# Performance work log

Measured on AMD Instinct MI355X. Metric: run time of the kernel, lower is better.

The kernel has to match this reference:

```python
import jax, jax.numpy as jnp
import numpy as np

D = 8        # q_ndim (= dof_ndim)
HID = 200    # hidden_size
N = 16384    # batch of states
EPS = 0.1    # qdot regularizer coefficient in L()


def _lagrangian(z, Ws, bs):
    # z: (2D,) = [q, qdot]; angular_dims=() so CosSin is an identity pass-through
    v = z[D:]
    h = z
    for W, b in zip(Ws[:-1], bs[:-1]):
        h = jax.nn.softplus(h @ W + b)   # FCsoftplus blocks
    L = (h @ Ws[-1] + bs[-1])[0]          # final Linear -> scalar (Reshape(-1))
    return L + EPS * jnp.dot(v, v)


def setup_inputs():
    key = jax.random.key(0)
    ks = jax.random.split(key, 5)
    z = jax.random.normal(ks[0], (N, 2 * D), dtype=jnp.float32)
    t = jnp.zeros((), dtype=jnp.float32)

    def lin(k, fi, fo, scale):
        return (jax.random.normal(k, (fi, fo), dtype=jnp.float32)
                * jnp.float32(scale / np.sqrt(fi)))

    W0 = lin(ks[1], 2 * D, HID, 1.0)
    W1 = lin(ks[2], HID, HID, 1.0)
    W2 = lin(ks[3], HID, HID, 1.0)
    W3 = lin(ks[4], HID, 1, 0.01)  # small head keeps mass matrix M well conditioned
    b0 = jnp.zeros((HID,), jnp.float32)  # zero_bias init per FCsoftplus/Linear
    b1 = jnp.zeros((HID,), jnp.float32)
    b2 = jnp.zeros((HID,), jnp.float32)
    b3 = jnp.zeros((1,), jnp.float32)
    return dict(t=t, z=z, W0=W0, b0=b0, W1=W1, b1=b1, W2=W2, b2=b2, W3=W3, b3=b3)


def reference(t, z, W0, b0, W1, b1, W2, b2, W3, b3):
    # Euler-Lagrange dynamics (LagrangianDynamics):
    #   M a = dL/dq - (d2L/dq dv) v,  M = d2L/dv2;  dz/dt = [v, a]
    Ws = (W0, W1, W2, W3)
    bs = (b0, b1, b2, b3)
    Lfn = lambda zz: _lagrangian(zz, Ws, bs)

    def dyn_single(zi):
        g = jax.grad(Lfn)(zi)              # (2D,)  = [dL/dq, dL/dv]
        H = jax.jacfwd(jax.grad(Lfn))(zi)  # (2D,2D) Hessian of L wrt z
        v = zi[D:]
        M = H[D:, D:]                      # d(dL/dv)/dv  -> mass matrix
        C = H[D:, :D]                      # d(dL/dv)/dq
        F = g[:D] - C @ v
        a = jnp.linalg.solve(M, F)
        return jnp.concatenate([v, a])     # (2D,)

    return jax.vmap(dyn_single)(z)         # (N, 2D)
```

## Files before the change

### kernel.cpp

```cpp
#include <hip/hip_runtime.h>
#include <math.h>

#define DD 8
#define ZD 16
#define HID 200
#define EPSL 0.1f
#define BS 8
#define NTHREADS 512
#define NKC 7
#define NMT 13
#define XSTR 200
#define CSTR 208
#define WSTR 208
#define NTAN 8
#define NT4 4

#define KSC 1024.0f
#define SSC 64.0f
#define INV_K (1.0f/1024.0f)
#define INV_KS (1.0f/65536.0f)

typedef _Float16 half8 __attribute__((ext_vector_type(8)));
typedef _Float16 half4v __attribute__((ext_vector_type(4)));
typedef _Float16 half2v __attribute__((ext_vector_type(2)));
typedef float float4v __attribute__((ext_vector_type(4)));

#define S4 (NKC*NMT*64*8)
#define OFF_W1T 0
#define OFF_W2T (S4)
#define OFF_W1  (2*S4)
#define OFF_W2  (3*S4)
#define OFF_W0T (4*S4)
#define OFF_W0  (4*S4 + NMT*64*8)
#define WS_HALFS (4*S4 + NMT*64*8 + NKC*64*8)

__global__ void prep(const float* __restrict__ W0, const float* __restrict__ W1,
                     const float* __restrict__ W2, _Float16* __restrict__ ws)
{
    int idx = blockIdx.x * 256 + threadIdx.x;
    if (idx >= WS_HALFS) return;
    float v = 0.f;
    if (idx < 4*S4) {
        int arr = idx / S4, e = idx % S4;
        int kc = e / (NMT*64*8); int r = e % (NMT*64*8);
        int mt = r / (64*8); r %= 64*8;
        int lane = r / 8, j = r % 8;
        int m = mt*16 + (lane & 15);
        int k = kc*32 + (lane >> 4)*8 + j;
        if (m < HID && k < HID) {
            if      (arr == 0) v = W1[k*HID + m];
            else if (arr == 1) v = W2[k*HID + m];
            else if (arr == 2) v = W1[m*HID + k];
            else               v = W2[m*HID + k];
        }
    } else if (idx < OFF_W0) {
        int e = idx - OFF_W0T;
        int mt = e / (64*8); int r = e % (64*8);
        int lane = r / 8, j = r % 8;
        int m = mt*16 + (lane & 15);
        int k = (lane >> 4)*8 + j;
        if (m < HID && k < ZD) v = W0[k*HID + m];
    } else {
        int e = idx - OFF_W0;
        int kc = e / (64*8); int r = e % (64*8);
        int lane = r / 8, j = r % 8;
        int m = (lane & 15);
        int k = kc*32 + (lane >> 4)*8 + j;
        if (k < HID) v = W0[m*HID + k];
    }
    ws[idx] = (_Float16)v;
}

__device__ __forceinline__ half4v pk4(float4v a) {
    half2v lo = __builtin_bit_cast(half2v, __builtin_amdgcn_cvt_pkrtz(a.x, a.y));
    half2v hi = __builtin_bit_cast(half2v, __builtin_amdgcn_cvt_pkrtz(a.z, a.w));
    return __builtin_shufflevector(lo, hi, 0, 1, 2, 3);
}
__device__ __forceinline__ void sig_sp(float x, float& sp, float& sg) {
    float e = __expf(-fabsf(x));
    float r = 1.0f / (1.0f + e);
    sg = (x >= 0.f) ? r : (1.0f - r);
    sp = fmaxf(x, 0.f) + __logf(1.f + e);
}

template<int NTILES, int MTC>
__device__ __forceinline__ void run_mv(const half8* __restrict__ Asw,
                                       const _Float16* __restrict__ Xsrc,
                                       int mt0, int lane,
                                       float4v acc[MTC][NTILES])
{
    const int lm = lane & 15, q = lane >> 4;
    constexpr int PF = (NTILES > 1) ? 2 : NKC;
#pragma unroll
    for (int m = 0; m < MTC; ++m)
#pragma unroll
        for (int n = 0; n < NTILES; ++n)
            acc[m][n] = (float4v){0.f, 0.f, 0.f, 0.f};

    half8 a[MTC][PF];
#pragma unroll
    for (int p = 0; p < PF; ++p)
#pragma unroll
        for (int m = 0; m < MTC; ++m)
            a[m][p] = Asw[(p*NMT + mt0 + m)*64 + lane];

#pragma unroll
    for (int kc = 0; kc < NKC; ++kc) {
        half8 x[NTILES];
#pragma unroll
        for (int n = 0; n < NTILES; ++n)
            x[n] = *(const half8*)(Xsrc + (n*16 + lm)*XSTR + kc*32 + q*8);
        half8 an[MTC];
        if (kc + PF < NKC)
#pragma unroll
            for (int m = 0; m < MTC; ++m)
                an[m] = Asw[((kc+PF)*NMT + mt0 + m)*64 + lane];
#pragma unroll
        for (int m = 0; m < MTC; ++m)
#pragma unroll
            for (int n = 0; n < NTILES; ++n)
                acc[m][n] = __builtin_amdgcn_mfma_f32_16x16x32_f16(a[m][0], x[n], acc[m][n], 0, 0, 0);
#pragma unroll
        for (int m = 0; m < MTC; ++m)
#pragma unroll
            for (int p = 0; p + 1 < PF; ++p) a[m][p] = a[m][p+1];
        if (kc + PF < NKC)
#pragma unroll
            for (int m = 0; m < MTC; ++m) a[m][PF-1] = an[m];
    }
}

__global__ void __launch_bounds__(NTHREADS, 4)
lnn_main(const float* __restrict__ z,
         const float* __restrict__ W0, const float* __restrict__ b0,
         const float* __restrict__ b1, const float* __restrict__ b2,
         const float* __restrict__ W3,
         const _Float16* __restrict__ ws,
         float* __restrict__ out)
{
    __shared__ alignas(16) _Float16 Xt[64*XSTR + 24];
    __shared__ alignas(16) _Float16 Xb[64*XSTR + 24];
    __shared__ alignas(16) _Float16 Cf[5][8*CSTR];
    __shared__ alignas(16) _Float16 Xz[16*32];
    __shared__ alignas(16) _Float16 bsh[4*WSTR];
    __shared__ alignas(16) _Float16 w0t[NTAN*WSTR];
    __shared__ alignas(16) float gsh[8*16];
    __shared__ alignas(16) float Hr[64*16];

    const int tid  = threadIdx.x;
    const int wave = tid >> 6;
    const int lane = tid & 63;
    const int lm   = lane & 15;
    const int q    = lane >> 4;
    const int s0   = blockIdx.x * BS;

    const int mt0 = (wave < 5) ? wave*2 : (10 + (wave - 5));
    const int mtc = (wave < 5) ? 2 : 1;

    const half8* W1Tsw = (const half8*)(ws + OFF_W1T);
    const half8* W2Tsw = (const half8*)(ws + OFF_W2T);
    const half8* W1sw  = (const half8*)(ws + OFF_W1);
    const half8* W2sw  = (const half8*)(ws + OFF_W2);
    const half8* W0Tsw = (const half8*)(ws + OFF_W0T);
    const half8* W0sw  = (const half8*)(ws + OFF_W0);

    for (int idx = tid; idx < 16*32; idx += NTHREADS) {
        int s = idx >> 5, c = idx & 31;
        Xz[idx] = (s < BS && c < ZD) ? (_Float16)z[(s0 + s)*ZD + c] : (_Float16)0.f;
    }
    if (tid < 24) {
        Xt[16*XSTR + tid] = (_Float16)0.f;
        Xb[16*XSTR + tid] = (_Float16)0.f;
        Xt[64*XSTR + tid] = (_Float16)0.f;
        Xb[64*XSTR + tid] = (_Float16)0.f;
    }
    for (int idx = tid; idx < 4*WSTR; idx += NTHREADS) {
        int l = idx / WSTR, u = idx % WSTR;
        float v = 0.f;
        if (u < HID) {
            if      (l == 0) v = b0[u];
            else if (l == 1) v = b1[u];
            else if (l == 2) v = b2[u];
            else             v = KSC * W3[u];
        }
        bsh[idx] = (_Float16)v;
    }
    for (int idx = tid; idx < NTAN*WSTR; idx += NTHREADS) {
        int t = idx / WSTR, u = idx % WSTR;
        w0t[idx] = (_Float16)((u < HID) ? SSC * W0[(DD + t)*HID + u] : 0.f);
    }
    __syncthreads();

    float4v acc1[2][1];

    {
        half8 xz = *(const half8*)(Xz + lm*32 + q*8);
#pragma unroll
        for (int m = 0; m < 2; ++m)
            if (m < mtc) {
                acc1[m][0] = (float4v){0.f,0.f,0.f,0.f};
                half8 a = W0Tsw[(mt0 + m)*64 + lane];
                acc1[m][0] = __builtin_amdgcn_mfma_f32_16x16x32_f16(a, xz, acc1[m][0], 0, 0, 0);
                const int ub = (mt0 + m)*16 + q*4;
                const bool padq = (mt0 + m == 12) && (q >= 2);
                half4v bb = *(const half4v*)(&bsh[0*WSTR + ub]);
                float h[4], p[4];
#pragma unroll
                for (int r = 0; r < 4; ++r) {
                    float av = acc1[m][0][r] + (float)bb[r];
                    sig_sp(av, h[r], p[r]);
                }
                if (!padq) *(half4v*)(&Xt[lm*XSTR + ub]) = pk4((float4v){h[0],h[1],h[2],h[3]});
                if (lm < BS) *(half4v*)(&Cf[0][lm*CSTR + ub]) = pk4((float4v){p[0],p[1],p[2],p[3]});
            }
    }
    __syncthreads();

    {
        if (mtc == 2) run_mv<1,2>(W1Tsw, Xt, mt0, lane, acc1);
        else          run_mv<1,1>(W1Tsw, Xt, mt0, lane, acc1);
#pragma unroll
        for (int m = 0; m < 2; ++m)
            if (m < mtc) {
                const int ub = (mt0 + m)*16 + q*4;
                const bool padq = (mt0 + m == 12) && (q >= 2);
                half4v bb = *(const half4v*)(&bsh[1*WSTR + ub]);
                float h[4], p[4];
#pragma unroll
                for (int r = 0; r < 4; ++r) {
                    float av = acc1[m][0][r] + (float)bb[r];
                    sig_sp(av, h[r], p[r]);
                }
                if (!padq) *(half4v*)(&Xb[lm*XSTR + ub]) = pk4((float4v){h[0],h[1],h[2],h[3]});
                if (lm < BS) *(half4v*)(&Cf[1][lm*CSTR + ub]) = pk4((float4v){p[0],p[1],p[2],p[3]});
            }
    }
    __syncthreads();

    {
        if (mtc == 2) run_mv<1,2>(W2Tsw, Xb, mt0, lane, acc1);
        else          run_mv<1,1>(W2Tsw, Xb, mt0, lane, acc1);
#pragma unroll
        for (int m = 0; m < 2; ++m)
            if (m < mtc) {
                const int ub = (mt0 + m)*16 + q*4;
                const bool padq = (mt0 + m == 12) && (q >= 2);
                half4v bb = *(const half4v*)(&bsh[2*WSTR + ub]);
                half4v w3 = *(const half4v*)(&bsh[3*WSTR + ub]);
                float d2[4], c2[4];
#pragma unroll
                for (int r = 0; r < 4; ++r) {
                    float av = acc1[m][0][r] + (float)bb[r];
                    float e = __expf(-fabsf(av));
                    float rr = 1.f / (1.f + e);
                    float sg = (av >= 0.f) ? rr : (1.f - rr);
                    float wk = (float)w3[r];
                    d2[r] = wk * sg;
                    c2[r] = wk * sg * (1.f - sg);
                }
                if (!padq) *(half4v*)(&Xt[lm*XSTR + ub]) = pk4((float4v){d2[0],d2[1],d2[2],d2[3]});
                if (lm < BS) *(half4v*)(&Cf[2][lm*CSTR + ub]) = pk4((float4v){c2[0],c2[1],c2[2],c2[3]});
            }
    }
    __syncthreads();

    {
        if (mtc == 2) run_mv<1,2>(W2sw, Xt, mt0, lane, acc1);
        else          run_mv<1,1>(W2sw, Xt, mt0, lane, acc1);
#pragma unroll
        for (int m = 0; m < 2; ++m)
            if (m < mtc) {
                const int ub = (mt0 + m)*16 + q*4;
                const bool padq = (mt0 + m == 12) && (q >= 2);
                half4v p1 = *(const half4v*)(&Cf[1][(lm & 7)*CSTR + ub]);
                half4v u1 = pk4(acc1[m][0]);
                half4v one = {(_Float16)1.f,(_Float16)1.f,(_Float16)1.f,(_Float16)1.f};
                if (!padq) *(half4v*)(&Xb[lm*XSTR + ub]) = u1 * p1;
                if (lm < BS) *(half4v*)(&Cf[3][lm*CSTR + ub]) = u1 * (one - p1);
            }
    }
    __syncthreads();

    {
        if (mtc == 2) run_mv<1,2>(W1sw, Xb, mt0, lane, acc1);
        else          run_mv<1,1>(W1sw, Xb, mt0, lane, acc1);
#pragma unroll
        for (int m = 0; m < 2; ++m)
            if (m < mtc) {
                const int ub = (mt0 + m)*16 + q*4;
                const bool padq = (mt0 + m == 12) && (q >= 2);
                half4v p0 = *(const half4v*)(&Cf[0][(lm & 7)*CSTR + ub]);
                half4v u0 = pk4(acc1[m][0]);
                half4v one = {(_Float16)1.f,(_Float16)1.f,(_Float16)1.f,(_Float16)1.f};
                half4v d0 = u0 * p0;
                if (!padq) *(half4v*)(&Xt[lm*XSTR + ub]) = d0;
                if (lm < BS) *(half4v*)(&Cf[4][lm*CSTR + ub]) = d0 * (one - p0);
            }
    }
    __syncthreads();

    if (wave == 0) {
        half8 aw[NKC];
#pragma unroll
        for (int kc = 0; kc < NKC; ++kc) aw[kc] = W0sw[kc*64 + lane];
        float4v g = (float4v){0.f,0.f,0.f,0.f};
#pragma unroll
        for (int kc = 0; kc < NKC; ++kc) {
            half8 x = *(const half8*)(Xt + lm*XSTR + kc*32 + q*8);
            g = __builtin_amdgcn_mfma_f32_16x16x32_f16(aw[kc], x, g, 0, 0, 0);
        }
        if (lm < BS) {
            float4v gv; gv.x = g.x*INV_K; gv.y = g.y*INV_K; gv.z = g.z*INV_K; gv.w = g.w*INV_K;
            *(float4v*)(&gsh[lm*16 + q*4]) = gv;
        }
    } else {
        for (int idx = tid - 64; idx < 64*50; idx += NTHREADS - 64) {
            int row = idx / 50, u = (idx % 50)*4;
            int s = row & 7, t = row >> 3;
            half4v p0 = *(const half4v*)(&Cf[0][s*CSTR + u]);
            half4v w0 = *(const half4v*)(&w0t[t*WSTR + u]);
            *(half4v*)(&Xb[row*XSTR + u]) = p0 * w0;
        }
    }
    __syncthreads();

    float4v acc4[2][NT4];
    half4v c3th1[2][NT4];

    {
        if (mtc == 2) run_mv<NT4,2>(W1Tsw, Xb, mt0, lane, acc4);
        else          run_mv<NT4,1>(W1Tsw, Xb, mt0, lane, acc4);
#pragma unroll
        for (int m = 0; m < 2; ++m)
            if (m < mtc) {
                const int ub = (mt0 + m)*16 + q*4;
                const bool padq = (mt0 + m == 12) && (q >= 2);
                half4v p1 = *(const half4v*)(&Cf[1][(lm & 7)*CSTR + ub]);
                half4v c3 = *(const half4v*)(&Cf[3][(lm & 7)*CSTR + ub]);
#pragma unroll
                for (int n = 0; n < NT4; ++n) {
                    half4v t = pk4(acc4[m][n]) * p1;
                    if (!padq) *(half4v*)(&Xt[(n*16 + lm)*XSTR + ub]) = t;
                    c3th1[m][n] = c3 * t;
                }
            }
    }
    __syncthreads();

    {
        if (mtc == 2) run_mv<NT4,2>(W2Tsw, Xt, mt0, lane, acc4);
        else          run_mv<NT4,1>(W2Tsw, Xt, mt0, lane, acc4);
#pragma unroll
        for (int m = 0; m < 2; ++m)
            if (m < mtc) {
                const int ub = (mt0 + m)*16 + q*4;
                const bool padq = (mt0 + m == 12) && (q >= 2);
                half4v c2 = *(const half4v*)(&Cf[2][(lm & 7)*CSTR + ub]);
#pragma unroll
                for (int n = 0; n < NT4; ++n)
                    if (!padq) *(half4v*)(&Xb[(n*16 + lm)*XSTR + ub]) = pk4(acc4[m][n]) * c2;
            }
    }
    __syncthreads();

    {
        if (mtc == 2) run_mv<NT4,2>(W2sw, Xb, mt0, lane, acc4);
        else          run_mv<NT4,1>(W2sw, Xb, mt0, lane, acc4);
#pragma unroll
        for (int m = 0; m < 2; ++m)
            if (m < mtc) {
                const int ub = (mt0 + m)*16 + q*4;
                const bool padq = (mt0 + m == 12) && (q >= 2);
                half4v p1 = *(const half4v*)(&Cf[1][(lm & 7)*CSTR + ub]);
#pragma unroll
                for (int n = 0; n < NT4; ++n)
                    if (!padq) *(half4v*)(&Xt[(n*16 + lm)*XSTR + ub]) = pk4(acc4[m][n]) * p1 + c3th1[m][n];
            }
    }
    __syncthreads();

    {
        if (mtc == 2) run_mv<NT4,2>(W1sw, Xt, mt0, lane, acc4);
        else          run_mv<NT4,1>(W1sw, Xt, mt0, lane, acc4);
#pragma unroll
        for (int m = 0; m < 2; ++m)
            if (m < mtc) {
                const int ub = (mt0 + m)*16 + q*4;
                const bool padq = (mt0 + m == 12) && (q >= 2);
                half4v p0 = *(const half4v*)(&Cf[0][(lm & 7)*CSTR + ub]);
                half4v c4 = *(const half4v*)(&Cf[4][(lm & 7)*CSTR + ub]);
#pragma unroll
                for (int n = 0; n < NT4; ++n) {
                    int t = n*2 + (lm >> 3);
                    half4v w0 = *(const half4v*)(&w0t[t*WSTR + ub]);
                    if (!padq) *(half4v*)(&Xb[(n*16 + lm)*XSTR + ub]) = pk4(acc4[m][n]) * p0 + c4 * w0;
                }
            }
    }
    __syncthreads();

    if (wave < 4) {
        half8 aw[NKC];
#pragma unroll
        for (int kc = 0; kc < NKC; ++kc) aw[kc] = W0sw[kc*64 + lane];
        float4v hacc = (float4v){0.f,0.f,0.f,0.f};
#pragma unroll
        for (int kc = 0; kc < NKC; ++kc) {
            half8 x = *(const half8*)(Xb + (wave*16 + lm)*XSTR + kc*32 + q*8);
            hacc = __builtin_amdgcn_mfma_f32_16x16x32_f16(aw[kc], x, hacc, 0, 0, 0);
        }
        int row = wave*16 + lm;
        float4v hv;
        hv.x = hacc.x*INV_KS; hv.y = hacc.y*INV_KS;
        hv.z = hacc.z*INV_KS; hv.w = hacc.w*INV_KS;
        *(float4v*)(&Hr[row*16 + q*4]) = hv;
    }
    __syncthreads();

    if (tid < BS) {
        const int s = tid;
        float M[DD][DD], F[DD], v[DD], a[DD];
#pragma unroll
        for (int c = 0; c < DD; ++c) v[c] = z[(s0 + s)*ZD + DD + c];
#pragma unroll
        for (int r = 0; r < DD; ++r) {
            float f = gsh[s*16 + r];
#pragma unroll
            for (int c = 0; c < DD; ++c) {
                M[r][c] = Hr[(r*8 + s)*16 + DD + c] + ((r == c) ? 2.f*EPSL : 0.f);
                f -= Hr[(r*8 + s)*16 + c] * v[c];
            }
            F[r] = f;
        }
#pragma unroll
        for (int col = 0; col < DD; ++col) {
            const float inv = 1.f / M[col][col];
#pragma unroll
            for (int r = col + 1; r < DD; ++r) {
                const float fac = M[r][col] * inv;
#pragma unroll
                for (int c = col + 1; c < DD; ++c) M[r][c] -= fac * M[col][c];
                F[r] -= fac * F[col];
            }
        }
#pragma unroll
        for (int r = DD - 1; r >= 0; --r) {
            float ssum = F[r];
#pragma unroll
            for (int c = r + 1; c < DD; ++c) ssum -= M[r][c] * a[c];
            a[r] = ssum / M[r][r];
        }
        float* op = out + (size_t)(s0 + s)*ZD;
#pragma unroll
        for (int c = 0; c < DD; ++c) { op[c] = v[c]; op[DD + c] = a[c]; }
    }
}

extern "C" void kernel_launch(void* const* d_in, const int* in_sizes, int n_in,
                              void* d_out, int out_size, void* d_ws, size_t ws_size,
                              hipStream_t stream)
{
    const float* z  = (const float*)d_in[1];
    const float* W0 = (const float*)d_in[2];
    const float* b0 = (const float*)d_in[3];
    const float* W1 = (const float*)d_in[4];
    const float* b1 = (const float*)d_in[5];
    const float* W2 = (const float*)d_in[6];
    const float* b2 = (const float*)d_in[7];
    const float* W3 = (const float*)d_in[8];
    float* out = (float*)d_out;
    _Float16* ws = (_Float16*)d_ws;

    const int n = in_sizes[1] / (2*DD);

    prep<<<dim3((WS_HALFS + 255)/256), dim3(256), 0, stream>>>(W0, W1, W2, ws);
    lnn_main<<<dim3(n / BS), dim3(NTHREADS), 0, stream>>>(
        z, W0, b0, b1, b2, W3, ws, out);
}
```

Before: 166.9 us.

## Split forward/backward pass and tangent pass into two kernels via global scratch

Splits the fused kernel into two. The first kernel runs the forward and gradient passes on 16 samples per block, so the 16-wide MFMA tiles are full instead of half padding. It writes the per-layer coefficient vectors (5×N×200 fp16) and the gradient to workspace. The second kernel reloads those coefficients and runs the Hessian tangent passes and the 8x8 solve for 8 samples per block. This trades wasted MFMA work for about 33 MB of extra global traffic plus a second launch. The old fused kernel remains as a fallback when the workspace is too small.

```diff
diff --git a/kernel.cpp b/kernel.cpp
--- a/kernel.cpp
+++ b/kernel.cpp
@@ -5,8 +5,6 @@
 #define ZD 16
 #define HID 200
 #define EPSL 0.1f
-#define BS 8
-#define NTHREADS 512
 #define NKC 7
 #define NMT 13
 #define XSTR 200
@@ -130,7 +128,365 @@
     }
 }
 
-__global__ void __launch_bounds__(NTHREADS, 4)
+__global__ void __launch_bounds__(512, 4)
+lnn_fwd(const float* __restrict__ z,
+        const float* __restrict__ b0, const float* __restrict__ b1,
+        const float* __restrict__ b2, const float* __restrict__ W3,
+        const _Float16* __restrict__ ws,
+        _Float16* __restrict__ cf, float* __restrict__ g, int N)
+{
+    __shared__ alignas(16) _Float16 Xa[16*XSTR + 24];
+    __shared__ alignas(16) _Float16 Xc[16*XSTR + 24];
+    __shared__ alignas(16) _Float16 CfF[2][16*CSTR];
+    __shared__ alignas(16) _Float16 Xz[16*32];
+    __shared__ alignas(16) _Float16 bsh[4*WSTR];
+
+    const int tid  = threadIdx.x;
+    const int wave = tid >> 6;
+    const int lane = tid & 63;
+    const int lm   = lane & 15;
+    const int q    = lane >> 4;
+    const int s0   = blockIdx.x * 16;
+
+    const int mt0 = (wave < 5) ? wave*2 : (10 + (wave - 5));
+    const int mtc = (wave < 5) ? 2 : 1;
+
+    const half8* W1Tsw = (const half8*)(ws + OFF_W1T);
+    const half8* W2Tsw = (const half8*)(ws + OFF_W2T);
+    const half8* W1sw  = (const half8*)(ws + OFF_W1);
+    const half8* W2sw  = (const half8*)(ws + OFF_W2);
+    const half8* W0Tsw = (const half8*)(ws + OFF_W0T);
+    const half8* W0sw  = (const half8*)(ws + OFF_W0);
+
+    {
+        int s = tid >> 5, c = tid & 31;
+        Xz[tid] = (c < ZD) ? (_Float16)z[(size_t)(s0 + s)*ZD + c] : (_Float16)0.f;
+    }
+    if (tid < 24) { Xa[16*XSTR + tid] = (_Float16)0.f; Xc[16*XSTR + tid] = (_Float16)0.f; }
+    for (int idx = tid; idx < 4*WSTR; idx += 512) {
+        int l = idx / WSTR, u = idx % WSTR;
+        float v = 0.f;
+        if (u < HID) {
+            if      (l == 0) v = b0[u];
+            else if (l == 1) v = b1[u];
+            else if (l == 2) v = b2[u];
+            else             v = KSC * W3[u];
+        }
+        bsh[idx] = (_Float16)v;
+    }
+    __syncthreads();
+
+    float4v acc1[2][1];
+
+    {
+        half8 xz = *(const half8*)(Xz + lm*32 + q*8);
+#pragma unroll
+        for (int m = 0; m < 2; ++m)
+            if (m < mtc) {
+                acc1[m][0] = (float4v){0.f,0.f,0.f,0.f};
+                half8 a = W0Tsw[(mt0 + m)*64 + lane];
+                acc1[m][0] = __builtin_amdgcn_mfma_f32_16x16x32_f16(a, xz, acc1[m][0], 0, 0, 0);
+                const int ub = (mt0 + m)*16 + q*4;
+                const bool padq = (mt0 + m == 12) && (q >= 2);
+                half4v bb = *(const half4v*)(&bsh[0*WSTR + ub]);
+                float h[4], p[4];
+#pragma unroll
+                for (int r = 0; r < 4; ++r) {
+                    float av = acc1[m][0][r] + (float)bb[r];
+                    sig_sp(av, h[r], p[r]);
+                }
+                half4v pp = pk4((float4v){p[0],p[1],p[2],p[3]});
+                if (!padq) *(half4v*)(&Xa[lm*XSTR + ub]) = pk4((float4v){h[0],h[1],h[2],h[3]});
+                *(half4v*)(&CfF[0][lm*CSTR + ub]) = pp;
+                if (!padq) *(half4v*)(cf + ((size_t)0*N + s0 + lm)*HID + ub) = pp;
+            }
+    }
+    __syncthreads();
+
+    {
+        if (mtc == 2) run_mv<1,2>(W1Tsw, Xa, mt0, lane, acc1);
+        else          run_mv<1,1>(W1Tsw, Xa, mt0, lane, acc1);
+#pragma unroll
+        for (int m = 0; m < 2; ++m)
+            if (m < mtc) {
+                const int ub = (mt0 + m)*16 + q*4;
+                const bool padq = (mt0 + m == 12) && (q >= 2);
+                half4v bb = *(const half4v*)(&bsh[1*WSTR + ub]);
+                float h[4], p[4];
+#pragma unroll
+                for (int r = 0; r < 4; ++r) {
+                    float av = acc1[m][0][r] + (float)bb[r];
+                    sig_sp(av, h[r], p[r]);
+                }
+                half4v pp = pk4((float4v){p[0],p[1],p[2],p[3]});
+                if (!padq) *(half4v*)(&Xc[lm*XSTR + ub]) = pk4((float4v){h[0],h[1],h[2],h[3]});
+                *(half4v*)(&CfF[1][lm*CSTR + ub]) = pp;
+                if (!padq) *(half4v*)(cf + ((size_t)1*N + s0 + lm)*HID + ub) = pp;
+            }
+    }
+    __syncthreads();
+
+    {
+        if (mtc == 2) run_mv<1,2>(W2Tsw, Xc, mt0, lane, acc1);
+        else          run_mv<1,1>(W2Tsw, Xc, mt0, lane, acc1);
+#pragma unroll
+        for (int m = 0; m < 2; ++m)
+            if (m < mtc) {
+                const int ub = (mt0 + m)*16 + q*4;
+                const bool padq = (mt0 + m == 12) && (q >= 2);
+                half4v bb = *(const half4v*)(&bsh[2*WSTR + ub]);
+                half4v w3 = *(const half4v*)(&bsh[3*WSTR + ub]);
+                float d2[4], c2[4];
+#pragma unroll
+                for (int r = 0; r < 4; ++r) {
+                    float av = acc1[m][0][r] + (float)bb[r];
+                    float e = __expf(-fabsf(av));
+                    float rr = 1.f / (1.f + e);
+                    float sg = (av >= 0.f) ? rr : (1.f - rr);
+                    float wk = (float)w3[r];
+                    d2[r] = wk * sg;
+                    c2[r] = wk * sg * (1.f - sg);
+                }
+                if (!padq) *(half4v*)(&Xa[lm*XSTR + ub]) = pk4((float4v){d2[0],d2[1],d2[2],d2[3]});
+                if (!padq) *(half4v*)(cf + ((size_t)2*N + s0 + lm)*HID + ub) = pk4((float4v){c2[0],c2[1],c2[2],c2[3]});
+            }
+    }
+    __syncthreads();
+
+    {
+        if (mtc == 2) run_mv<1,2>(W2sw, Xa, mt0, lane, acc1);
+        else          run_mv<1,1>(W2sw, Xa, mt0, lane, acc1);
+#pragma unroll
+        for (int m = 0; m < 2; ++m)
+            if (m < mtc) {
+                const int ub = (mt0 + m)*16 + q*4;
+                const bool padq = (mt0 + m == 12) && (q >= 2);
+                half4v p1 = *(const half4v*)(&CfF[1][lm*CSTR + ub]);
+                half4v u1 = pk4(acc1[m][0]);
+                half4v one = {(_Float16)1.f,(_Float16)1.f,(_Float16)1.f,(_Float16)1.f};
+                if (!padq) *(half4v*)(&Xc[lm*XSTR + ub]) = u1 * p1;
+                if (!padq) *(half4v*)(cf + ((size_t)3*N + s0 + lm)*HID + ub) = u1 * (one - p1);
+            }
+    }
+    __syncthreads();
+
+    {
+        if (mtc == 2) run_mv<1,2>(W1sw, Xc, mt0, lane, acc1);
+        else          run_mv<1,1>(W1sw, Xc, mt0, lane, acc1);
+#pragma unroll
+        for (int m = 0; m < 2; ++m)
+            if (m < mtc) {
+                const int ub = (mt0 + m)*16 + q*4;
+                const bool padq = (mt0 + m == 12) && (q >= 2);
+                half4v p0 = *(const half4v*)(&CfF[0][lm*CSTR + ub]);
+                half4v u0 = pk4(acc1[m][0]);
+                half4v one = {(_Float16)1.f,(_Float16)1.f,(_Float16)1.f,(_Float16)1.f};
+                half4v d0 = u0 * p0;
+                if (!padq) *(half4v*)(&Xa[lm*XSTR + ub]) = d0;
+                if (!padq) *(half4v*)(cf + ((size_t)4*N + s0 + lm)*HID + ub) = d0 * (one - p0);
+            }
+    }
+    __syncthreads();
+
+    if (wave == 0) {
+        half8 aw[NKC];
+#pragma unroll
+        for (int kc = 0; kc < NKC; ++kc) aw[kc] = W0sw[kc*64 + lane];
+        float4v gv = (float4v){0.f,0.f,0.f,0.f};
+#pragma unroll
+        for (int kc = 0; kc < NKC; ++kc) {
+            half8 x = *(const half8*)(Xa + lm*XSTR + kc*32 + q*8);
+            gv = __builtin_amdgcn_mfma_f32_16x16x32_f16(aw[kc], x, gv, 0, 0, 0);
+        }
+        float4v go; go.x = gv.x*INV_K; go.y = gv.y*INV_K; go.z = gv.z*INV_K; go.w = gv.w*INV_K;
+        *(float4v*)(g + (size_t)(s0 + lm)*16 + q*4) = go;
+    }
+}
+
+__global__ void __launch_bounds__(512, 4)
+lnn_tan(const float* __restrict__ z, const float* __restrict__ W0,
+        const _Float16* __restrict__ ws, const _Float16* __restrict__ cf,
+        const float* __restrict__ g, float* __restrict__ out, int N)
+{
+    __shared__ alignas(16) _Float16 Xt[64*XSTR + 24];
+    __shared__ alignas(16) _Float16 Xb[64*XSTR + 24];
+    __shared__ alignas(16) _Float16 Cf[5][8*CSTR];
+    __shared__ alignas(16) _Float16 w0t[NTAN*WSTR];
+    __shared__ alignas(16) float HrS[64*16];
+
+    const int tid  = threadIdx.x;
+    const int wave = tid >> 6;
+    const int lane = tid & 63;
+    const int lm   = lane & 15;
+    const int q    = lane >> 4;
+    const int s0   = blockIdx.x * 8;
+
+    const int mt0 = (wave < 5) ? wave*2 : (10 + (wave - 5));
+    const int mtc = (wave < 5) ? 2 : 1;
+
+    const half8* W1Tsw = (const half8*)(ws + OFF_W1T);
+    const half8* W2Tsw = (const half8*)(ws + OFF_W2T);
+    const half8* W1sw  = (const half8*)(ws + OFF_W1);
+    const half8* W2sw  = (const half8*)(ws + OFF_W2);
+    const half8* W0sw  = (const half8*)(ws + OFF_W0);
+
+    {
+        _Float16* cfl = &Cf[0][0];
+        for (int idx = tid; idx < 5*8*CSTR; idx += 512) {
+            int c = idx / (8*CSTR), r = idx % (8*CSTR);
+            int s = r / CSTR, u = r % CSTR;
+            cfl[idx] = (u < HID) ? cf[((size_t)c*N + s0 + s)*HID + u] : (_Float16)0.f;
+        }
+    }
+    for (int idx = tid; idx < NTAN*WSTR; idx += 512) {
+        int t = idx / WSTR, u = idx % WSTR;
+        w0t[idx] = (_Float16)((u < HID) ? SSC * W0[(size_t)(DD + t)*HID + u] : 0.f);
+    }
+    if (tid < 24) { Xt[64*XSTR + tid] = (_Float16)0.f; Xb[64*XSTR + tid] = (_Float16)0.f; }
+    __syncthreads();
+
+    for (int idx = tid; idx < 64*50; idx += 512) {
+        int row = idx / 50, u = (idx % 50)*4;
+        int s = row & 7, t = row >> 3;
+        half4v p0 = *(const half4v*)(&Cf[0][s*CSTR + u]);
+        half4v w0 = *(const half4v*)(&w0t[t*WSTR + u]);
+        *(half4v*)(&Xb[row*XSTR + u]) = p0 * w0;
+    }
+    __syncthreads();
+
+    float4v acc4[2][NT4];
+    half4v c3th1[2][NT4];
+
+    {
+        if (mtc == 2) run_mv<NT4,2>(W1Tsw, Xb, mt0, lane, acc4);
+        else          run_mv<NT4,1>(W1Tsw, Xb, mt0, lane, acc4);
+#pragma unroll
+        for (int m = 0; m < 2; ++m)
+            if (m < mtc) {
+                const int ub = (mt0 + m)*16 + q*4;
+                const bool padq = (mt0 + m == 12) && (q >= 2);
+                half4v p1 = *(const half4v*)(&Cf[1][(lm & 7)*CSTR + ub]);
+                half4v c3 = *(const half4v*)(&Cf[3][(lm & 7)*CSTR + ub]);
+#pragma unroll
+                for (int n = 0; n < NT4; ++n) {
+                    half4v t = pk4(acc4[m][n]) * p1;
+                    if (!padq) *(half4v*)(&Xt[(n*16 + lm)*XSTR + ub]) = t;
+                    c3th1[m][n] = c3 * t;
+                }
+            }
+    }
+    __syncthreads();
+
+    {
+        if (mtc == 2) run_mv<NT4,2>(W2Tsw, Xt, mt0, lane, acc4);
+        else          run_mv<NT4,1>(W2Tsw, Xt, mt0, lane, acc4);
+#pragma unroll
+        for (int m = 0; m < 2; ++m)
+            if (m < mtc) {
+                const int ub = (mt0 + m)*16 + q*4;
+                const bool padq = (mt0 + m == 12) && (q >= 2);
+                half4v c2 = *(const half4v*)(&Cf[2][(lm & 7)*CSTR + ub]);
+#pragma unroll
+                for (int n = 0; n < NT4; ++n)
+                    if (!padq) *(half4v*)(&Xb[(n*16 + lm)*XSTR + ub]) = pk4(acc4[m][n]) * c2;
+            }
+    }
+    __syncthreads();
+
+    {
+        if (mtc == 2) run_mv<NT4,2>(W2sw, Xb, mt0, lane, acc4);
+        else          run_mv<NT4,1>(W2sw, Xb, mt0, lane, acc4);
+#pragma unroll
+        for (int m = 0; m < 2; ++m)
+            if (m < mtc) {
+                const int ub = (mt0 + m)*16 + q*4;
+                const bool padq = (mt0 + m == 12) && (q >= 2);
+                half4v p1 = *(const half4v*)(&Cf[1][(lm & 7)*CSTR + ub]);
+#pragma unroll
+                for (int n = 0; n < NT4; ++n)
+                    if (!padq) *(half4v*)(&Xt[(n*16 + lm)*XSTR + ub]) = pk4(acc4[m][n]) * p1 + c3th1[m][n];
+            }
+    }
+    __syncthreads();
+
+    {
+        if (mtc == 2) run_mv<NT4,2>(W1sw, Xt, mt0, lane, acc4);
+        else          run_mv<NT4,1>(W1sw, Xt, mt0, lane, acc4);
+#pragma unroll
+        for (int m = 0; m < 2; ++m)
+            if (m < mtc) {
+                const int ub = (mt0 + m)*16 + q*4;
+                const bool padq = (mt0 + m == 12) && (q >= 2);
+                half4v p0 = *(const half4v*)(&Cf[0][(lm & 7)*CSTR + ub]);
+                half4v c4 = *(const half4v*)(&Cf[4][(lm & 7)*CSTR + ub]);
+#pragma unroll
+                for (int n = 0; n < NT4; ++n) {
+                    int t = n*2 + (lm >> 3);
+                    half4v w0 = *(const half4v*)(&w0t[t*WSTR + ub]);
+                    if (!padq) *(half4v*)(&Xb[(n*16 + lm)*XSTR + ub]) = pk4(acc4[m][n]) * p0 + c4 * w0;
+                }
+            }
+    }
+    __syncthreads();
+
+    if (wave < 4) {
+        half8 aw[NKC];
+#pragma unroll
+        for (int kc = 0; kc < NKC; ++kc) aw[kc] = W0sw[kc*64 + lane];
+        float4v hacc = (float4v){0.f,0.f,0.f,0.f};
+#pragma unroll
+        for (int kc = 0; kc < NKC; ++kc) {
+            half8 x = *(const half8*)(Xb + (wave*16 + lm)*XSTR + kc*32 + q*8);
+            hacc = __builtin_amdgcn_mfma_f32_16x16x32_f16(aw[kc], x, hacc, 0, 0, 0);
+        }
+        int row = wave*16 + lm;
+        float4v hv;
+        hv.x = hacc.x*INV_KS; hv.y = hacc.y*INV_KS;
+        hv.z = hacc.z*INV_KS; hv.w = hacc.w*INV_KS;
+        *(float4v*)(&HrS[row*16 + q*4]) = hv;
+    }
+    __syncthreads();
+
+    if (tid < 8) {
+        const int s = tid;
+        float M[DD][DD], F[DD], v[DD], a[DD];
+#pragma unroll
+        for (int c = 0; c < DD; ++c) v[c] = z[(size_t)(s0 + s)*ZD + DD + c];
+#pragma unroll
+        for (int r = 0; r < DD; ++r) {
+            float f = g[(size_t)(s0 + s)*16 + r];
+#pragma unroll
+            for (int c = 0; c < DD; ++c) {
+                M[r][c] = HrS[(r*8 + s)*16 + DD + c] + ((r == c) ? 2.f*EPSL : 0.f);
+                f -= HrS[(r*8 + s)*16 + c] * v[c];
+            }
+            F[r] = f;
+        }
+#pragma unroll
+        for (int col = 0; col < DD; ++col) {
+            const float inv = 1.f / M[col][col];
+#pragma unroll
+            for (int r = col + 1; r < DD; ++r) {
+                const float fac = M[r][col] * inv;
+#pragma unroll
+                for (int c = col + 1; c < DD; ++c) M[r][c] -= fac * M[col][c];
+                F[r] -= fac * F[col];
+            }
+        }
+#pragma unroll
+        for (int r = DD - 1; r >= 0; --r) {
+            float ssum = F[r];
+#pragma unroll
+            for (int c = r + 1; c < DD; ++c) ssum -= M[r][c] * a[c];
+            a[r] = ssum / M[r][r];
+        }
+        float* op = out + (size_t)(s0 + s)*ZD;
+#pragma unroll
+        for (int c = 0; c < DD; ++c) { op[c] = v[c]; op[DD + c] = a[c]; }
+    }
+}
+
+__global__ void __launch_bounds__(512, 4)
 lnn_main(const float* __restrict__ z,
          const float* __restrict__ W0, const float* __restrict__ b0,
          const float* __restrict__ b1, const float* __restrict__ b2,
@@ -152,7 +508,7 @@
     const int lane = tid & 63;
     const int lm   = lane & 15;
     const int q    = lane >> 4;
-    const int s0   = blockIdx.x * BS;
+    const int s0   = blockIdx.x * 8;
 
     const int mt0 = (wave < 5) ? wave*2 : (10 + (wave - 5));
     const int mtc = (wave < 5) ? 2 : 1;
@@ -164,9 +520,9 @@
     const half8* W0Tsw = (const half8*)(ws + OFF_W0T);
     const half8* W0sw  = (const half8*)(ws + OFF_W0);
 
-    for (int idx = tid; idx < 16*32; idx += NTHREADS) {
+    for (int idx = tid; idx < 16*32; idx += 512) {
         int s = idx >> 5, c = idx & 31;
-        Xz[idx] = (s < BS && c < ZD) ? (_Float16)z[(s0 + s)*ZD + c] : (_Float16)0.f;
+        Xz[idx] = (s < 8 && c < ZD) ? (_Float16)z[(s0 + s)*ZD + c] : (_Float16)0.f;
     }
     if (tid < 24) {
         Xt[16*XSTR + tid] = (_Float16)0.f;
@@ -174,7 +530,7 @@
         Xt[64*XSTR + tid] = (_Float16)0.f;
         Xb[64*XSTR + tid] = (_Float16)0.f;
     }
-    for (int idx = tid; idx < 4*WSTR; idx += NTHREADS) {
+    for (int idx = tid; idx < 4*WSTR; idx += 512) {
         int l = idx / WSTR, u = idx % WSTR;
         float v = 0.f;
         if (u < HID) {
@@ -185,7 +541,7 @@
         }
         bsh[idx] = (_Float16)v;
     }
-    for (int idx = tid; idx < NTAN*WSTR; idx += NTHREADS) {
+    for (int idx = tid; idx < NTAN*WSTR; idx += 512) {
         int t = idx / WSTR, u = idx % WSTR;
         w0t[idx] = (_Float16)((u < HID) ? SSC * W0[(DD + t)*HID + u] : 0.f);
     }
@@ -211,7 +567,7 @@
                     sig_sp(av, h[r], p[r]);
                 }
                 if (!padq) *(half4v*)(&Xt[lm*XSTR + ub]) = pk4((float4v){h[0],h[1],h[2],h[3]});
-                if (lm < BS) *(half4v*)(&Cf[0][lm*CSTR + ub]) = pk4((float4v){p[0],p[1],p[2],p[3]});
+                if (lm < 8) *(half4v*)(&Cf[0][lm*CSTR + ub]) = pk4((float4v){p[0],p[1],p[2],p[3]});
             }
     }
     __syncthreads();
@@ -232,7 +588,7 @@
                     sig_sp(av, h[r], p[r]);
                 }
                 if (!padq) *(half4v*)(&Xb[lm*XSTR + ub]) = pk4((float4v){h[0],h[1],h[2],h[3]});
-                if (lm < BS) *(half4v*)(&Cf[1][lm*CSTR + ub]) = pk4((float4v){p[0],p[1],p[2],p[3]});
+                if (lm < 8) *(half4v*)(&Cf[1][lm*CSTR + ub]) = pk4((float4v){p[0],p[1],p[2],p[3]});
             }
     }
     __syncthreads();
@@ -259,7 +615,7 @@
                     c2[r] = wk * sg * (1.f - sg);
                 }
                 if (!padq) *(half4v*)(&Xt[lm*XSTR + ub]) = pk4((float4v){d2[0],d2[1],d2[2],d2[3]});
-                if (lm < BS) *(half4v*)(&Cf[2][lm*CSTR + ub]) = pk4((float4v){c2[0],c2[1],c2[2],c2[3]});
+                if (lm < 8) *(half4v*)(&Cf[2][lm*CSTR + ub]) = pk4((float4v){c2[0],c2[1],c2[2],c2[3]});
             }
     }
     __syncthreads();
@@ -276,7 +632,7 @@
                 half4v u1 = pk4(acc1[m][0]);
                 half4v one = {(_Float16)1.f,(_Float16)1.f,(_Float16)1.f,(_Float16)1.f};
                 if (!padq) *(half4v*)(&Xb[lm*XSTR + ub]) = u1 * p1;
-                if (lm < BS) *(half4v*)(&Cf[3][lm*CSTR + ub]) = u1 * (one - p1);
+                if (lm < 8) *(half4v*)(&Cf[3][lm*CSTR + ub]) = u1 * (one - p1);
             }
     }
     __syncthreads();
@@ -294,7 +650,7 @@
                 half4v one = {(_Float16)1.f,(_Float16)1.f,(_Float16)1.f,(_Float16)1.f};
                 half4v d0 = u0 * p0;
                 if (!padq) *(half4v*)(&Xt[lm*XSTR + ub]) = d0;
-                if (lm < BS) *(half4v*)(&Cf[4][lm*CSTR + ub]) = d0 * (one - p0);
+                if (lm < 8) *(half4v*)(&Cf[4][lm*CSTR + ub]) = d0 * (one - p0);
             }
     }
     __syncthreads();
@@ -303,18 +659,18 @@
         half8 aw[NKC];
 #pragma unroll
         for (int kc = 0; kc < NKC; ++kc) aw[kc] = W0sw[kc*64 + lane];
-        float4v g = (float4v){0.f,0.f,0.f,0.f};
+        float4v gv = (float4v){0.f,0.f,0.f,0.f};
 #pragma unroll
         for (int kc = 0; kc < NKC; ++kc) {
             half8 x = *(const half8*)(Xt + lm*XSTR + kc*32 + q*8);
-            g = __builtin_amdgcn_mfma_f32_16x16x32_f16(aw[kc], x, g, 0, 0, 0);
-        }
-        if (lm < BS) {
-            float4v gv; gv.x = g.x*INV_K; gv.y = g.y*INV_K; gv.z = g.z*INV_K; gv.w = g.w*INV_K;
-            *(float4v*)(&gsh[lm*16 + q*4]) = gv;
+            gv = __builtin_amdgcn_mfma_f32_16x16x32_f16(aw[kc], x, gv, 0, 0, 0);
+        }
+        if (lm < 8) {
+            float4v go; go.x = gv.x*INV_K; go.y = gv.y*INV_K; go.z = gv.z*INV_K; go.w = gv.w*INV_K;
+            *(float4v*)(&gsh[lm*16 + q*4]) = go;
         }
     } else {
-        for (int idx = tid - 64; idx < 64*50; idx += NTHREADS - 64) {
+        for (int idx = tid - 64; idx < 64*50; idx += 512 - 64) {
             int row = idx / 50, u = (idx % 50)*4;
             int s = row & 7, t = row >> 3;
             half4v p0 = *(const half4v*)(&Cf[0][s*CSTR + u]);
@@ -417,7 +773,7 @@
     }
     __syncthreads();
 
-    if (tid < BS) {
+    if (tid < 8) {
         const int s = tid;
         float M[DD][DD], F[DD], v[DD], a[DD];
 #pragma unroll
@@ -474,6 +830,18 @@
     const int n = in_sizes[1] / (2*DD);
 
     prep<<<dim3((WS_HALFS + 255)/256), dim3(256), 0, stream>>>(W0, W1, W2, ws);
-    lnn_main<<<dim3(n / BS), dim3(NTHREADS), 0, stream>>>(
-        z, W0, b0, b1, b2, W3, ws, out);
+
+    const size_t w_bytes = (size_t)WS_HALFS * 2;
+    const size_t g_bytes = (size_t)n * 16 * 4;
+    const size_t cf_bytes = (size_t)5 * n * HID * 2;
+    const size_t need = w_bytes + g_bytes + cf_bytes;
+
+    if (ws_size >= need && (n % 16) == 0) {
+        float* g = (float*)((char*)d_ws + w_bytes);
+        _Float16* cf = (_Float16*)((char*)d_ws + w_bytes + g_bytes);
+        lnn_fwd<<<dim3(n / 16), dim3(512), 0, stream>>>(z, b0, b1, b2, W3, ws, cf, g, n);
+        lnn_tan<<<dim3(n / 8), dim3(512), 0, stream>>>(z, W0, ws, cf, g, out, n);
+    } else {
+        lnn_main<<<dim3(n / 8), dim3(512), 0, stream>>>(z, W0, b0, b1, b2, W3, ws, out);
+    }
 }
```

After: 183.4 us. 1.1x slower.
